# Kernel tuning notes

Hardware: AMD Instinct MI355X
Metric: run time of the kernel (lower is better)

Reference implementation:

```python
import jax, jax.numpy as jnp
from jax import lax
import numpy as np

D_MODEL = 1024
D_STATE = 64
D_CONV = 4
EXPAND = 2
HEADDIM = 64
D_INNER = EXPAND * D_MODEL          # 2048
NHEADS = D_INNER // HEADDIM         # 32
CHUNK = 64
CONV_DIM = D_INNER + 2 * D_STATE    # 2176
D_IN_PROJ = 2 * D_INNER + 2 * D_STATE + NHEADS  # 4256
B_SZ = 4
SEQLEN = 2048
EPS = 1e-5


def _silu(x):
    return x * jax.nn.sigmoid(x)


def _segsum(x):
    # x: [..., T]; returns [..., T, T] with [i,j] = sum_{j<k<=i} x[k], -inf above diag
    T = x.shape[-1]
    xe = jnp.broadcast_to(x[..., None], x.shape + (T,))
    strict_lower = jnp.tril(jnp.ones((T, T), bool), -1)
    xe = jnp.where(strict_lower, xe, 0.0)
    s = jnp.cumsum(xe, axis=-2)
    lower = jnp.tril(jnp.ones((T, T), bool), 0)
    return jnp.where(lower, s, -jnp.inf)


def setup_inputs() -> dict:
    key = jax.random.key(0)
    ks = jax.random.split(key, 5)
    u = jax.random.normal(ks[0], (B_SZ, SEQLEN, D_MODEL), jnp.float32)
    W_in = jax.random.normal(ks[1], (D_IN_PROJ, D_MODEL), jnp.float32) * 0.02
    conv_w = jax.random.normal(ks[2], (CONV_DIM, 1, D_CONV), jnp.float32) * 0.2  # depthwise kernel
    conv_b = jnp.zeros((CONV_DIM,), jnp.float32)
    dt_bias = jax.random.uniform(ks[3], (NHEADS,), jnp.float32, -1.0, 1.0)
    A_log = jnp.log(jnp.linspace(1.0, float(NHEADS), NHEADS)).astype(jnp.float32)
    D = jnp.ones((NHEADS,), jnp.float32)
    norm_w = jnp.ones((D_INNER,), jnp.float32)
    W_out = jax.random.normal(ks[4], (D_MODEL, D_INNER), jnp.float32) * 0.02
    return dict(u=u, W_in=W_in, conv_w=conv_w, conv_b=conv_b, dt_bias=dt_bias,
                A_log=A_log, D=D, norm_w=norm_w, W_out=W_out)


def reference(u, W_in, conv_w, conv_b, dt_bias, A_log, D, norm_w, W_out):
    b, s, _ = u.shape
    A = -jnp.exp(A_log)                                   # [H]
    zxbcdt = u @ W_in.T                                   # [b,s,D_IN_PROJ]
    z = zxbcdt[..., :D_INNER]
    xBC = zxbcdt[..., D_INNER:D_INNER + CONV_DIM]
    dt = jax.nn.softplus(zxbcdt[..., D_INNER + CONV_DIM:] + dt_bias)  # [b,s,H]

    # causal depthwise conv1d (left pad d_conv-1 == torch pad-both + slice[:s])
    xc = lax.conv_general_dilated(
        xBC.transpose(0, 2, 1), conv_w, window_strides=(1,),
        padding=[(D_CONV - 1, 0)], feature_group_count=CONV_DIM,
        dimension_numbers=('NCH', 'OIH', 'NCH'))
    xBC = _silu(xc.transpose(0, 2, 1) + conv_b)           # [b,s,CONV_DIM]

    x = xBC[..., :D_INNER].reshape(b, s, NHEADS, HEADDIM)
    Bm = xBC[..., D_INNER:D_INNER + D_STATE]              # [b,s,N]
    Cm = xBC[..., D_INNER + D_STATE:]                     # [b,s,N]

    # SSD chunked scan
    nch = s // CHUNK
    xs = (x * dt[..., None]).reshape(b, nch, CHUNK, NHEADS, HEADDIM)
    Ad = (A * dt).reshape(b, nch, CHUNK, NHEADS)
    Br = Bm.reshape(b, nch, CHUNK, D_STATE)
    Cr = Cm.reshape(b, nch, CHUNK, D_STATE)
    A_ch = Ad.transpose(0, 1, 3, 2)                       # [b,c,h,l]
    A_cum = jnp.cumsum(A_ch, axis=-1)
    L = jnp.exp(_segsum(A_ch))                            # [b,c,h,l,l]
    Y_diag = jnp.einsum('bcln,bcsn,bchls,bcshp->bclhp', Cr, Br, L, xs)
    decay_states = jnp.exp(A_cum[..., -1:] - A_cum)       # [b,c,h,l]
    states = jnp.einsum('bchl,bcln,bclhp->bchpn', decay_states, Br, xs)
    init = jnp.zeros((b, 1, NHEADS, HEADDIM, D_STATE), xs.dtype)
    states = jnp.concatenate([init, states], axis=1)      # [b,c+1,h,p,n]
    total_decay = jnp.pad(A_cum[..., -1].transpose(0, 2, 1), ((0, 0), (0, 0), (1, 0)))
    decay_chunk = jnp.exp(_segsum(total_decay))           # [b,h,c+1,c+1]
    new_states = jnp.einsum('bhzc,bchpn->bzhpn', decay_chunk, states)
    states = new_states[:, :-1]                           # [b,c,h,p,n]
    state_decay_out = jnp.exp(A_cum)
    Y_off = jnp.einsum('bcln,bchpn,bchl->bclhp', Cr, states, state_decay_out)
    y = (Y_diag + Y_off).reshape(b, s, NHEADS, HEADDIM)

    y = y + x * D[:, None]
    y = y.reshape(b, s, D_INNER)
    # gated RMSNorm
    y = y * _silu(z)
    y = y * lax.rsqrt(jnp.mean(y * y, axis=-1, keepdims=True) + EPS) * norm_w
    return y @ W_out.T
```

## Files before the change

kernel.cpp:

```cpp
#include <hip/hip_runtime.h>
#include <hip/hip_bf16.h>

#define BSZ 4
#define SEQ 2048
#define DMODEL 1024
#define DINNER 2048
#define DSTATE 64
#define NH 32
#define HD 64
#define CKL 64
#define NCH 32
#define CONVD 2176
#define DPROJ 4256
#define N1 4224
#define MTOT 8192
#define YSTR 72

typedef __hip_bfloat16 bf16;
typedef __attribute__((ext_vector_type(8))) short short8;
typedef __attribute__((ext_vector_type(4))) short short4_;
typedef __attribute__((ext_vector_type(4))) float f32x4;

__device__ __forceinline__ float sigmoidf_(float x) { return 1.0f / (1.0f + __expf(-x)); }
__device__ __forceinline__ float bits2f(short s) { return __uint_as_float(((unsigned)(unsigned short)s) << 16); }
__device__ __forceinline__ short f2bits(float f) {
    bf16 h = __float2bfloat16(f);
    return *reinterpret_cast<short*>(&h);
}

__device__ __forceinline__ void gl_lds16(const bf16* g, bf16* l) {
    __builtin_amdgcn_global_load_lds((const __attribute__((address_space(1))) void*)g,
                                     (__attribute__((address_space(3))) void*)l, 16, 0, 0);
}

__device__ __forceinline__ void swz8(int& bx, int& by) {
    int nx = gridDim.x;
    int L = blockIdx.y * nx + blockIdx.x;
    int GSZ = nx * 8;
    int g = L / GSZ, r = L - g * GSZ;
    bx = r % nx;
    by = g * 8 + r / nx;
}

__global__ void k_cvt2(const float* __restrict__ W_in, const float* __restrict__ W_out,
                       const float* __restrict__ nw, bf16* __restrict__ win_b,
                       bf16* __restrict__ wout_b) {
    int g = (blockIdx.x * 256 + threadIdx.x) * 4;
    if (g < N1 * DMODEL) {
        f32x4 f = *(const f32x4*)&W_in[g];
        short4_ o;
#pragma unroll
        for (int j = 0; j < 4; j++) o[j] = f2bits(f[j]);
        *(short4_*)&win_b[g] = o;
    } else if (g < N1 * DMODEL + DMODEL * DINNER) {
        int g2 = g - N1 * DMODEL;
        f32x4 f = *(const f32x4*)&W_out[g2];
        f32x4 w = *(const f32x4*)&nw[g2 & (DINNER - 1)];
        short4_ o;
#pragma unroll
        for (int j = 0; j < 4; j++) o[j] = f2bits(f[j] * w[j]);
        *(short4_*)&wout_b[g2] = o;
    }
}

__global__ __launch_bounds__(256) void k_gemm_bt(const bf16* __restrict__ A, const bf16* __restrict__ W,
                                                 bf16* __restrict__ C, int N, int K, int lda) {
    __shared__ __align__(16) bf16 lA[128 * 64];
    __shared__ __align__(16) bf16 lB[128 * 64];
    const int tid = threadIdx.x;
    const int lane = tid & 63, w = tid >> 6;
    const int wm = w >> 1, wn = w & 1;
    const int lr = lane & 15, lk = lane >> 4;
    int bx, by;
    swz8(bx, by);
    const int m0 = by * 128, n0 = bx * 128;

    f32x4 acc[4][4];
#pragma unroll
    for (int i = 0; i < 4; i++)
#pragma unroll
        for (int j = 0; j < 4; j++) acc[i][j] = (f32x4){0.f, 0.f, 0.f, 0.f};

    const int r = tid >> 3;
    const int cs = ((tid & 7) ^ (r & 7)) * 8;
    const bf16* ga = A + (size_t)(m0 + r) * lda + cs;
    const bf16* gb = W + (size_t)(n0 + r) * K + cs;
    bf16* la0 = lA + tid * 8;
    bf16* lb0 = lB + tid * 8;
    const int sx = (lr & 7);

    for (int kt = 0; kt < K; kt += 64) {
#pragma unroll
        for (int i = 0; i < 4; i++) {
            gl_lds16(ga + kt + (size_t)(32 * i) * lda, la0 + 2048 * i);
            gl_lds16(gb + kt + (size_t)(32 * i) * K, lb0 + 2048 * i);
        }
        __syncthreads();
#pragma unroll
        for (int hh = 0; hh < 2; hh++) {
            const int cb = ((lk + 4 * hh) ^ sx) * 8;
            short8 af[4], bfr[4];
#pragma unroll
            for (int im = 0; im < 4; im++)
                af[im] = *(const short8*)&lA[(wm * 64 + im * 16 + lr) * 64 + cb];
#pragma unroll
            for (int jn = 0; jn < 4; jn++)
                bfr[jn] = *(const short8*)&lB[(wn * 64 + jn * 16 + lr) * 64 + cb];
#pragma unroll
            for (int im = 0; im < 4; im++)
#pragma unroll
                for (int jn = 0; jn < 4; jn++)
                    acc[im][jn] = __builtin_amdgcn_mfma_f32_16x16x32_bf16(af[im], bfr[jn], acc[im][jn], 0, 0, 0);
        }
        __syncthreads();
    }
#pragma unroll
    for (int im = 0; im < 4; im++) {
        int row = m0 + wm * 64 + im * 16 + lk * 4;
#pragma unroll
        for (int jn = 0; jn < 4; jn++) {
            int col = n0 + wn * 64 + jn * 16 + lr;
            bf16* cp = C + (size_t)row * N + col;
#pragma unroll
            for (int rr = 0; rr < 4; rr++) cp[(size_t)rr * N] = __float2bfloat16(acc[im][jn][rr]);
        }
    }
}

__global__ __launch_bounds__(256) void k_gemm2(const bf16* __restrict__ A, const bf16* __restrict__ W,
                                               float* __restrict__ C) {
    __shared__ __align__(16) bf16 lA[128 * 64];
    __shared__ __align__(16) bf16 lB[128 * 64];
    __shared__ float rsrow[128];
    const int tid = threadIdx.x;
    const int lane = tid & 63, w = tid >> 6;
    const int wm = w >> 1, wn = w & 1;
    const int lr = lane & 15, lk = lane >> 4;
    int bx, by;
    swz8(bx, by);
    const int m0 = by * 128, n0 = bx * 128;
    const int K = DINNER, N = DMODEL;

    f32x4 acc[4][4];
#pragma unroll
    for (int i = 0; i < 4; i++)
#pragma unroll
        for (int j = 0; j < 4; j++) acc[i][j] = (f32x4){0.f, 0.f, 0.f, 0.f};
    float ssq[4] = {0.f, 0.f, 0.f, 0.f};

    const int r = tid >> 3;
    const int cs = ((tid & 7) ^ (r & 7)) * 8;
    const bf16* ga = A + (size_t)(m0 + r) * N1 + cs;
    const bf16* gb = W + (size_t)(n0 + r) * K + cs;
    bf16* la0 = lA + tid * 8;
    bf16* lb0 = lB + tid * 8;
    const int sx = (lr & 7);

    for (int kt = 0; kt < K; kt += 64) {
#pragma unroll
        for (int i = 0; i < 4; i++) {
            gl_lds16(ga + kt + (size_t)(32 * i) * N1, la0 + 2048 * i);
            gl_lds16(gb + kt + (size_t)(32 * i) * K, lb0 + 2048 * i);
        }
        __syncthreads();
#pragma unroll
        for (int hh = 0; hh < 2; hh++) {
            const int cb = ((lk + 4 * hh) ^ sx) * 8;
            short8 af[4], bfr[4];
#pragma unroll
            for (int im = 0; im < 4; im++) {
                af[im] = *(const short8*)&lA[(wm * 64 + im * 16 + lr) * 64 + cb];
#pragma unroll
                for (int j = 0; j < 8; j++) { float v = bits2f(af[im][j]); ssq[im] += v * v; }
            }
#pragma unroll
            for (int jn = 0; jn < 4; jn++)
                bfr[jn] = *(const short8*)&lB[(wn * 64 + jn * 16 + lr) * 64 + cb];
#pragma unroll
            for (int im = 0; im < 4; im++)
#pragma unroll
                for (int jn = 0; jn < 4; jn++)
                    acc[im][jn] = __builtin_amdgcn_mfma_f32_16x16x32_bf16(af[im], bfr[jn], acc[im][jn], 0, 0, 0);
        }
        __syncthreads();
    }
#pragma unroll
    for (int im = 0; im < 4; im++) {
        float s = ssq[im];
        s += __shfl_down(s, 32);
        s += __shfl_down(s, 16);
        if (lane < 16) rsrow[wm * 64 + im * 16 + lane] = rsqrtf(s * (1.0f / DINNER) + 1e-5f);
    }
    __syncthreads();
#pragma unroll
    for (int im = 0; im < 4; im++) {
        int rloc = wm * 64 + im * 16 + lk * 4;
        int row = m0 + rloc;
#pragma unroll
        for (int rr = 0; rr < 4; rr++) {
            float s = rsrow[rloc + rr];
#pragma unroll
            for (int jn = 0; jn < 4; jn++) {
                int col = n0 + wn * 64 + jn * 16 + lr;
                C[(size_t)(row + rr) * N + col] = acc[im][jn][rr] * s;
            }
        }
    }
}

__global__ __launch_bounds__(256) void k_prep(const float* __restrict__ u, const float* __restrict__ W_in,
                                              const float* __restrict__ dt_bias,
                                              bf16* __restrict__ u_b, float* __restrict__ dtt) {
    __shared__ __align__(16) float us[8 * DMODEL];
    const int t0 = blockIdx.x * 8;
    const int tid = threadIdx.x;
    const float* ur = u + (size_t)t0 * DMODEL;
    bf16* ub = u_b + (size_t)t0 * DMODEL;
#pragma unroll
    for (int i = 0; i < 8; i++) {
        int idx = (i * 256 + tid) * 4;
        f32x4 v = *(const f32x4*)&ur[idx];
        *(f32x4*)&us[idx] = v;
        short4_ o;
#pragma unroll
        for (int j = 0; j < 4; j++) o[j] = f2bits(v[j]);
        *(short4_*)&ub[idx] = o;
    }
    __syncthreads();
    const int h = tid >> 3, sub = tid & 7;
    const float* wr = W_in + (size_t)(DPROJ - NH + h) * DMODEL;
    float s[8] = {};
    for (int k = sub * 4; k < DMODEL; k += 32) {
        f32x4 w4 = *(const f32x4*)&wr[k];
#pragma unroll
        for (int rr = 0; rr < 8; rr++) {
            const float* up = &us[rr * DMODEL + k];
            s[rr] += up[0] * w4[0] + up[1] * w4[1] + up[2] * w4[2] + up[3] * w4[3];
        }
    }
#pragma unroll
    for (int rr = 0; rr < 8; rr++) {
        s[rr] += __shfl_down(s[rr], 4, 8);
        s[rr] += __shfl_down(s[rr], 2, 8);
        s[rr] += __shfl_down(s[rr], 1, 8);
    }
    if (sub == 0) {
        float bh = dt_bias[h];
#pragma unroll
        for (int rr = 0; rr < 8; rr++) {
            float x = s[rr] + bh;
            dtt[(size_t)h * MTOT + t0 + rr] = (x > 20.f) ? x : log1pf(__expf(x));
        }
    }
}

__global__ void k_conv(const bf16* __restrict__ zx, const float* __restrict__ cw,
                       const float* __restrict__ cb, bf16* __restrict__ xbc) {
    int g = (blockIdx.x * 256 + threadIdx.x) * 4;
    if (g >= MTOT * CONVD) return;
    int c0 = g % CONVD;
    int t = g / CONVD;
    int s = t & (SEQ - 1);
    const short* base = (const short*)(zx + (size_t)t * N1 + DINNER + c0);
    f32x4 w0 = *(const f32x4*)&cw[(c0 + 0) * 4];
    f32x4 w1 = *(const f32x4*)&cw[(c0 + 1) * 4];
    f32x4 w2 = *(const f32x4*)&cw[(c0 + 2) * 4];
    f32x4 w3 = *(const f32x4*)&cw[(c0 + 3) * 4];
    f32x4 a = *(const f32x4*)&cb[c0];
#pragma unroll
    for (int k = 0; k < 4; k++) {
        int st = s - 3 + k;
        if (st >= 0) {
            short4_ v = *(const short4_*)(base + (long)(k - 3) * N1);
            a[0] += bits2f(v[0]) * w0[k];
            a[1] += bits2f(v[1]) * w1[k];
            a[2] += bits2f(v[2]) * w2[k];
            a[3] += bits2f(v[3]) * w3[k];
        }
    }
    short4_ o;
#pragma unroll
    for (int j = 0; j < 4; j++) o[j] = f2bits(a[j] * sigmoidf_(a[j]));
    *(short4_*)&xbc[g] = o;
}

__global__ __launch_bounds__(256) void k_ssd(const bf16* __restrict__ xbc, const float* __restrict__ dtt,
                                             const float* __restrict__ A_log, const float* __restrict__ Dp,
                                             bf16* __restrict__ zx) {
    __shared__ __align__(16) short Ct[2][64 * YSTR];
    __shared__ __align__(16) short Bt[2][64 * YSTR];
    __shared__ __align__(16) short Bn[2][64 * YSTR];
    __shared__ __align__(16) short Xt[2][32 * YSTR];
    __shared__ __align__(16) short Sb[2][32 * YSTR];
    __shared__ __align__(16) short Gs[4 * 16 * YSTR];
    __shared__ __align__(16) float Sf[32 * 68];
    __shared__ __align__(16) float sdt2[2][64], sAc2[2][64], sf2[2][64];
    __shared__ float set2[2];

    const int ph = blockIdx.x, h = blockIdx.y, b = blockIdx.z;
    const int tid = threadIdx.x;
    const int lane = tid & 63, w = tid >> 6;
    const int lr = lane & 15, lk = lane >> 4;
    const float Ah = -__expf(A_log[h]);
    const float Dh = Dp[h];
    const int xcol = h * HD + ph * 32;

    const int lrow = tid >> 2, c0 = (tid & 3) * 16, px = (tid & 3) * 8;
    const int zl = 16 * w + (lane >> 2), zp = (lane & 3) * 8;

    short8 rC0, rC1, rB0, rB1, rX, rZ;
    float rdt;
    auto load_chunk = [&](int cc) {
        int rows0 = b * SEQ + cc * CKL;
        const short* rp = (const short*)(xbc + (size_t)(rows0 + lrow) * CONVD);
        rC0 = *(const short8*)&rp[DINNER + DSTATE + c0];
        rC1 = *(const short8*)&rp[DINNER + DSTATE + c0 + 8];
        rB0 = *(const short8*)&rp[DINNER + c0];
        rB1 = *(const short8*)&rp[DINNER + c0 + 8];
        rX  = *(const short8*)&rp[xcol + px];
        rZ  = *(const short8*)((const short*)zx + (size_t)(rows0 + zl) * N1 + xcol + zp);
        rdt = dtt[(size_t)h * MTOT + rows0 + lane];
    };
    auto scatter = [&](int buf) {
        *(short8*)&Ct[buf][lrow * YSTR + c0] = rC0;
        *(short8*)&Ct[buf][lrow * YSTR + c0 + 8] = rC1;
        *(short8*)&Bt[buf][lrow * YSTR + c0] = rB0;
        *(short8*)&Bt[buf][lrow * YSTR + c0 + 8] = rB1;
#pragma unroll
        for (int j = 0; j < 8; j++) {
            Bn[buf][(c0 + j) * YSTR + lrow] = rB0[j];
            Bn[buf][(c0 + 8 + j) * YSTR + lrow] = rB1[j];
            Xt[buf][(px + j) * YSTR + lrow] = rX[j];
        }
    };
    auto dtscan = [&](int buf) {
        if (tid < 64) {
            float dv = rdt;
            float v = Ah * dv;
#pragma unroll
            for (int d = 1; d < 64; d <<= 1) { float o = __shfl_up(v, d); if (tid >= d) v += o; }
            float tot = __shfl(v, 63);
            sdt2[buf][tid] = dv; sAc2[buf][tid] = v; sf2[buf][tid] = __expf(tot - v) * dv;
            if (tid == 63) set2[buf] = __expf(tot);
        }
    };

    for (int i = tid; i < 32 * 68; i += 256) Sf[i] = 0.f;
    for (int i = tid; i < 32 * YSTR; i += 256) Sb[0][i] = 0;
    load_chunk(0);
    scatter(0);
    dtscan(0);
    __syncthreads();

    for (int c = 0; c < NCH; c++) {
        const int par = c & 1, nb = par ^ 1;
        const int rows0 = b * SEQ + c * CKL;
        float etot = set2[par];
        short8 zcur = rZ;
        if (c + 1 < NCH) load_chunk(c + 1);

        short8 cf0 = *(const short8*)&Ct[par][(16 * w + lr) * YSTR + lk * 8];
        short8 cf1 = *(const short8*)&Ct[par][(16 * w + lr) * YSTR + 32 + lk * 8];
        f32x4 acc[2];
#pragma unroll
        for (int t = 0; t < 2; t++) {
            short8 s0 = *(const short8*)&Sb[par][(16 * t + lr) * YSTR + lk * 8];
            short8 s1 = *(const short8*)&Sb[par][(16 * t + lr) * YSTR + 32 + lk * 8];
            acc[t] = __builtin_amdgcn_mfma_f32_16x16x32_bf16(cf0, s0, (f32x4){0.f, 0.f, 0.f, 0.f}, 0, 0, 0);
            acc[t] = __builtin_amdgcn_mfma_f32_16x16x32_bf16(cf1, s1, acc[t], 0, 0, 0);
        }
        float sAcl[4], el[4];
#pragma unroll
        for (int rr = 0; rr < 4; rr++) { sAcl[rr] = sAc2[par][16 * w + lk * 4 + rr]; el[rr] = __expf(sAcl[rr]); }
#pragma unroll
        for (int t = 0; t < 2; t++)
#pragma unroll
            for (int rr = 0; rr < 4; rr++) acc[t][rr] *= el[rr];
        short* gw = Gs + w * 16 * YSTR;
#pragma unroll
        for (int t = 0; t < 4; t++) {
            short8 b0 = *(const short8*)&Bt[par][(16 * t + lr) * YSTR + lk * 8];
            short8 b1 = *(const short8*)&Bt[par][(16 * t + lr) * YSTR + 32 + lk * 8];
            f32x4 g = __builtin_amdgcn_mfma_f32_16x16x32_bf16(cf0, b0, (f32x4){0.f, 0.f, 0.f, 0.f}, 0, 0, 0);
            g = __builtin_amdgcn_mfma_f32_16x16x32_bf16(cf1, b1, g, 0, 0, 0);
            int s = 16 * t + lr;
            float sAcs = sAc2[par][s], dts = sdt2[par][s];
#pragma unroll
            for (int rr = 0; rr < 4; rr++) {
                int l = 16 * w + lk * 4 + rr;
                float v = (s <= l) ? g[rr] * __expf(sAcl[rr] - sAcs) * dts : 0.f;
                gw[(lk * 4 + rr) * YSTR + s] = f2bits(v);
            }
        }
        short8 gf0 = *(const short8*)&gw[lr * YSTR + lk * 8];
        short8 gf1 = *(const short8*)&gw[lr * YSTR + 32 + lk * 8];
#pragma unroll
        for (int t = 0; t < 2; t++) {
            short8 x0 = *(const short8*)&Xt[par][(16 * t + lr) * YSTR + lk * 8];
            short8 x1 = *(const short8*)&Xt[par][(16 * t + lr) * YSTR + 32 + lk * 8];
            acc[t] = __builtin_amdgcn_mfma_f32_16x16x32_bf16(gf0, x0, acc[t], 0, 0, 0);
            acc[t] = __builtin_amdgcn_mfma_f32_16x16x32_bf16(gf1, x1, acc[t], 0, 0, 0);
        }
        {
            int pw = w & 1, nh2 = w >> 1;
            short8 xt0 = *(const short8*)&Xt[par][(16 * pw + lr) * YSTR + lk * 8];
            short8 xt1 = *(const short8*)&Xt[par][(16 * pw + lr) * YSTR + 32 + lk * 8];
            f32x4 sa0 = *(const f32x4*)&sf2[par][lk * 8];
            f32x4 sa1 = *(const f32x4*)&sf2[par][lk * 8 + 4];
            f32x4 sb0 = *(const f32x4*)&sf2[par][32 + lk * 8];
            f32x4 sb1 = *(const f32x4*)&sf2[par][32 + lk * 8 + 4];
            short8 xd0, xd1;
#pragma unroll
            for (int j = 0; j < 4; j++) {
                xd0[j]     = f2bits(bits2f(xt0[j])     * sa0[j]);
                xd0[4 + j] = f2bits(bits2f(xt0[4 + j]) * sa1[j]);
                xd1[j]     = f2bits(bits2f(xt1[j])     * sb0[j]);
                xd1[4 + j] = f2bits(bits2f(xt1[4 + j]) * sb1[j]);
            }
#pragma unroll
            for (int j = 0; j < 2; j++) {
                int nt = 2 * nh2 + j;
                short8 b0 = *(const short8*)&Bn[par][(16 * nt + lr) * YSTR + lk * 8];
                short8 b1 = *(const short8*)&Bn[par][(16 * nt + lr) * YSTR + 32 + lk * 8];
                f32x4 sacc = __builtin_amdgcn_mfma_f32_16x16x32_bf16(xd0, b0, (f32x4){0.f, 0.f, 0.f, 0.f}, 0, 0, 0);
                sacc = __builtin_amdgcn_mfma_f32_16x16x32_bf16(xd1, b1, sacc, 0, 0, 0);
#pragma unroll
                for (int rr = 0; rr < 4; rr++) {
                    int n = 16 * nt + lr;
                    int p = 16 * pw + lk * 4 + rr;
                    float nv = Sf[p * 68 + n] * etot + sacc[rr];
                    Sf[p * 68 + n] = nv;
                    Sb[nb][p * YSTR + n] = f2bits(nv);
                }
            }
        }
#pragma unroll
        for (int t = 0; t < 2; t++) {
#pragma unroll
            for (int rr = 0; rr < 4; rr++) {
                int p = 16 * t + lr;
                int l = 16 * w + lk * 4 + rr;
                float y = acc[t][rr] + Dh * bits2f(Xt[par][p * YSTR + l]);
                Ct[par][l * YSTR + p] = f2bits(y);
            }
        }
        {
            short8 y8 = *(const short8*)&Ct[par][zl * YSTR + zp];
            short* zpp = (short*)zx + (size_t)(rows0 + zl) * N1 + xcol + zp;
            short8 o;
#pragma unroll
            for (int j = 0; j < 8; j++) {
                float z = bits2f(zcur[j]);
                o[j] = f2bits(bits2f(y8[j]) * (z * sigmoidf_(z)));
            }
            *(short8*)zpp = o;
        }
        if (c + 1 < NCH) {
            scatter(nb);
            dtscan(nb);
        }
        __syncthreads();
    }
}

extern "C" void kernel_launch(void* const* d_in, const int* in_sizes, int n_in,
                              void* d_out, int out_size, void* d_ws, size_t ws_size,
                              hipStream_t stream) {
    const float* u       = (const float*)d_in[0];
    const float* W_in    = (const float*)d_in[1];
    const float* conv_w  = (const float*)d_in[2];
    const float* conv_b  = (const float*)d_in[3];
    const float* dt_bias = (const float*)d_in[4];
    const float* A_log   = (const float*)d_in[5];
    const float* Dp      = (const float*)d_in[6];
    const float* norm_w  = (const float*)d_in[7];
    const float* W_out   = (const float*)d_in[8];
    float* out = (float*)d_out;

    char* ws = (char*)d_ws;
    bf16* zx     = (bf16*)ws;  ws += (size_t)MTOT * N1 * 2;
    bf16* xbc    = (bf16*)ws;  ws += (size_t)MTOT * CONVD * 2;
    bf16* wout_b = (bf16*)ws;  ws += (size_t)DMODEL * DINNER * 2;
    float* dtt   = (float*)ws; ws += (size_t)NH * MTOT * 4;

    bf16* u_b   = (bf16*)d_out;
    bf16* win_b = (bf16*)((char*)d_out + (size_t)MTOT * DMODEL * 2);

    k_prep<<<MTOT / 8, 256, 0, stream>>>(u, W_in, dt_bias, u_b, dtt);
    k_cvt2<<<((N1 * DMODEL + DMODEL * DINNER) / 4 + 255) / 256, 256, 0, stream>>>(
        W_in, W_out, norm_w, win_b, wout_b);

    k_gemm_bt<<<dim3(N1 / 128, MTOT / 128), 256, 0, stream>>>(u_b, win_b, zx, N1, DMODEL, DMODEL);

    k_conv<<<(MTOT * CONVD / 4 + 255) / 256, 256, 0, stream>>>(zx, conv_w, conv_b, xbc);

    k_ssd<<<dim3(2, NH, BSZ), 256, 0, stream>>>(xbc, dtt, A_log, Dp, zx);

    k_gemm2<<<dim3(DMODEL / 128, MTOT / 128), 256, 0, stream>>>(zx, wout_b, out);
}
```

Measured before the change: 407.7 us.

## Replace both GEMMs with 8-wave double-buffered pipelined MFMA template kernel

Replaces the two 128x128 single-buffered GEMM kernels with one templated 512-thread kernel. It uses wider N tiles (384 for the input projection, 256 for the output projection), double-buffered LDS split into half-K stages, and async global-to-LDS loads issued ahead of compute with explicit vmcnt waits. MFMA clusters run under raised priority with sched barriers, and the tile order changes to an XCD-aware block remap. The goal is to hide global load latency and raise MFMA utilisation. In exchange it brings larger LDS use, hand-tuned wait counts that are easy to get wrong, and fewer blocks per GEMM.

```diff
diff --git a/kernel.cpp b/kernel.cpp
--- a/kernel.cpp
+++ b/kernel.cpp
@@ -33,13 +33,26 @@
                                      (__attribute__((address_space(3))) void*)l, 16, 0, 0);
 }
 
-__device__ __forceinline__ void swz8(int& bx, int& by) {
-    int nx = gridDim.x;
-    int L = blockIdx.y * nx + blockIdx.x;
-    int GSZ = nx * 8;
-    int g = L / GSZ, r = L - g * GSZ;
-    bx = r % nx;
-    by = g * 8 + r / nx;
+__device__ __forceinline__ f32x4 MF(short8 a, short8 b, f32x4 c) {
+    return __builtin_amdgcn_mfma_f32_16x16x32_bf16(a, b, c, 0, 0, 0);
+}
+
+template<int N> __device__ __forceinline__ void vmw() {
+    if constexpr (N < 0) {}
+    else if constexpr (N == 0)  asm volatile("s_waitcnt vmcnt(0)" ::: "memory");
+    else if constexpr (N == 1)  asm volatile("s_waitcnt vmcnt(1)" ::: "memory");
+    else if constexpr (N == 2)  asm volatile("s_waitcnt vmcnt(2)" ::: "memory");
+    else if constexpr (N == 3)  asm volatile("s_waitcnt vmcnt(3)" ::: "memory");
+    else if constexpr (N == 4)  asm volatile("s_waitcnt vmcnt(4)" ::: "memory");
+    else if constexpr (N == 5)  asm volatile("s_waitcnt vmcnt(5)" ::: "memory");
+    else if constexpr (N == 6)  asm volatile("s_waitcnt vmcnt(6)" ::: "memory");
+    else if constexpr (N == 7)  asm volatile("s_waitcnt vmcnt(7)" ::: "memory");
+    else if constexpr (N == 8)  asm volatile("s_waitcnt vmcnt(8)" ::: "memory");
+    else if constexpr (N == 9)  asm volatile("s_waitcnt vmcnt(9)" ::: "memory");
+    else if constexpr (N == 10) asm volatile("s_waitcnt vmcnt(10)" ::: "memory");
+    else if constexpr (N == 11) asm volatile("s_waitcnt vmcnt(11)" ::: "memory");
+    else if constexpr (N == 12) asm volatile("s_waitcnt vmcnt(12)" ::: "memory");
+    else                        asm volatile("s_waitcnt vmcnt(15)" ::: "memory");
 }
 
 __global__ void k_cvt2(const float* __restrict__ W_in, const float* __restrict__ W_out,
@@ -63,146 +76,171 @@
     }
 }
 
-__global__ __launch_bounds__(256) void k_gemm_bt(const bf16* __restrict__ A, const bf16* __restrict__ W,
-                                                 bf16* __restrict__ C, int N, int K, int lda) {
-    __shared__ __align__(16) bf16 lA[128 * 64];
-    __shared__ __align__(16) bf16 lB[128 * 64];
+template<int BN, int NT, int LDA, int LDC, bool RMS, typename CT>
+__global__ __launch_bounds__(512, 2) void k_mm8(const bf16* __restrict__ Ap,
+                                                const bf16* __restrict__ Wp,
+                                                CT* __restrict__ Cp) {
+    constexpr int K   = NT * 64;
+    constexpr int NJ  = BN / 64;
+    constexpr int WNW = BN / 4;
+    constexpr int LB  = BN / 128;
+    constexpr int SBH = BN * 32;
+    constexpr int WS  = 3 * LB + 2;
+
+    __shared__ __align__(16) short SA[16384];
+    __shared__ __align__(16) short SB[4 * SBH];
+    __shared__ float rsrow[RMS ? 128 : 1];
+
     const int tid = threadIdx.x;
     const int lane = tid & 63, w = tid >> 6;
-    const int wm = w >> 1, wn = w & 1;
+    const int wm = w >> 2, wn = w & 3;
     const int lr = lane & 15, lk = lane >> 4;
-    int bx, by;
-    swz8(bx, by);
-    const int m0 = by * 128, n0 = bx * 128;
-
-    f32x4 acc[4][4];
+
+    const int NX = gridDim.x;
+    {
+    }
+    int L = blockIdx.y * NX + blockIdx.x;
+    int nwg = NX * gridDim.y;
+    int Lx = (L & 7) * (nwg >> 3) + (L >> 3);
+    const int m0 = (Lx / NX) * 128, n0 = (Lx % NX) * BN;
+
+    const int la = tid >> 2;
+    const int rA = (la & ~5) | ((la & 1) << 2) | ((la >> 2) & 1);
+    const bf16* pA = Ap + (size_t)(m0 + rA) * LDA + (((tid & 3) ^ (rA & 3)) * 8);
+    const bf16* pB[LB];
+#pragma unroll
+    for (int q = 0; q < LB; q++) {
+        int lb = (w * LB + q) * 16 + (lane >> 2);
+        int rB = (lb & ~5) | ((lb & 1) << 2) | ((lb >> 2) & 1);
+        pB[q] = Wp + (size_t)(n0 + rB) * K + (((lane & 3) ^ (rB & 3)) * 8);
+    }
+
+    auto stA = [&](int d, int h, int t) {
+        gl_lds16(pA + t * 64 + h * 32, (bf16*)&SA[(d * 2 + h) * 4096 + tid * 8]);
+    };
+    auto stB = [&](int d, int h, int t) {
+#pragma unroll
+        for (int q = 0; q < LB; q++)
+            gl_lds16(pB[q] + t * 64 + h * 32,
+                     (bf16*)&SB[(d * 2 + h) * SBH + (w * LB + q) * 512 + lane * 8]);
+    };
+
+    const int lnsw = (lr & 10) | ((lr & 1) << 2) | ((lr >> 2) & 1);
+    const int pe = (lk ^ (lr & 3)) * 8;
+    const int aBase = (wm * 64 + lnsw) * 32 + pe;
+    const int bBase = (wn * WNW + lnsw) * 32 + pe;
+
+    f32x4 acc[4][NJ];
 #pragma unroll
     for (int i = 0; i < 4; i++)
 #pragma unroll
-        for (int j = 0; j < 4; j++) acc[i][j] = (f32x4){0.f, 0.f, 0.f, 0.f};
-
-    const int r = tid >> 3;
-    const int cs = ((tid & 7) ^ (r & 7)) * 8;
-    const bf16* ga = A + (size_t)(m0 + r) * lda + cs;
-    const bf16* gb = W + (size_t)(n0 + r) * K + cs;
-    bf16* la0 = lA + tid * 8;
-    bf16* lb0 = lB + tid * 8;
-    const int sx = (lr & 7);
-
-    for (int kt = 0; kt < K; kt += 64) {
+        for (int j = 0; j < NJ; j++) acc[i][j] = (f32x4){0.f, 0.f, 0.f, 0.f};
+    float ssq[4] = {0.f, 0.f, 0.f, 0.f};
+
+#define CLUSTER(I0, I1)                                              \
+    do {                                                             \
+        __builtin_amdgcn_s_barrier();                                \
+        asm volatile("s_waitcnt lgkmcnt(0)" ::: "memory");           \
+        __builtin_amdgcn_sched_barrier(0);                           \
+        __builtin_amdgcn_s_setprio(1);                               \
+        _Pragma("unroll")                                            \
+        for (int j = 0; j < NJ; ++j) {                               \
+            acc[I0][j] = MF(af[0], bfr[j], acc[I0][j]);              \
+            acc[I1][j] = MF(af[1], bfr[j], acc[I1][j]);              \
+        }                                                            \
+        __builtin_amdgcn_s_setprio(0);                               \
+    } while (0)
+
+#define SSQ2(I0, I1)                                                 \
+    if constexpr (RMS) {                                             \
+        _Pragma("unroll")                                            \
+        for (int e = 0; e < 8; ++e) {                                \
+            float v0 = bits2f(af[0][e]), v1 = bits2f(af[1][e]);      \
+            ssq[I0] += v0 * v0; ssq[I1] += v1 * v1;                  \
+        }                                                            \
+    }
+
+    stB(0, 0, 0); stA(0, 0, 0); stB(0, 1, 0); stA(0, 1, 0);
+    stB(1, 0, 1); stA(1, 0, 1); stB(1, 1, 1);
+    vmw<WS>();
+    __builtin_amdgcn_s_barrier();
+
+#pragma unroll
+    for (int t = 0; t < NT; ++t) {
+        const int d = t & 1;
+        const int A0 = d * 8192, A1 = A0 + 4096;
+        const int B0 = d * 2 * SBH, B1 = B0 + SBH;
+        short8 af[2], bfr[NJ];
+#pragma unroll
+        for (int j = 0; j < NJ; ++j) bfr[j] = *(const short8*)&SB[B0 + bBase + j * 512];
+        af[0] = *(const short8*)&SA[A0 + aBase];
+        af[1] = *(const short8*)&SA[A0 + aBase + 512];
+        if (t + 1 < NT) stA(d ^ 1, 1, t + 1);
+        CLUSTER(0, 1);
+        SSQ2(0, 1);
+        __builtin_amdgcn_s_barrier();
+        af[0] = *(const short8*)&SA[A0 + aBase + 1024];
+        af[1] = *(const short8*)&SA[A0 + aBase + 1536];
+        if (t + 2 < NT) stB(d, 0, t + 2);
+        CLUSTER(2, 3);
+        SSQ2(2, 3);
+        if (t < NT - 2) vmw<WS>();
+        else if (t == NT - 2) vmw<2 * LB + 2>();
+        else vmw<0>();
+        __builtin_amdgcn_s_barrier();
+#pragma unroll
+        for (int j = 0; j < NJ; ++j) bfr[j] = *(const short8*)&SB[B1 + bBase + j * 512];
+        af[0] = *(const short8*)&SA[A1 + aBase];
+        af[1] = *(const short8*)&SA[A1 + aBase + 512];
+        if (t + 2 < NT) stA(d, 0, t + 2);
+        CLUSTER(0, 1);
+        SSQ2(0, 1);
+        __builtin_amdgcn_s_barrier();
+        af[0] = *(const short8*)&SA[A1 + aBase + 1024];
+        af[1] = *(const short8*)&SA[A1 + aBase + 1536];
+        if (t + 2 < NT) stB(d, 1, t + 2);
+        CLUSTER(2, 3);
+        SSQ2(2, 3);
+        if (t < NT - 2) vmw<WS>();
+        else if (t == NT - 2) vmw<LB + 1>();
+        __builtin_amdgcn_s_barrier();
+    }
+#undef CLUSTER
+#undef SSQ2
+
+    if constexpr (RMS) {
 #pragma unroll
         for (int i = 0; i < 4; i++) {
-            gl_lds16(ga + kt + (size_t)(32 * i) * lda, la0 + 2048 * i);
-            gl_lds16(gb + kt + (size_t)(32 * i) * K, lb0 + 2048 * i);
+            float s = ssq[i];
+            s += __shfl_down(s, 32);
+            s += __shfl_down(s, 16);
+            if (lane < 16) rsrow[wm * 64 + i * 16 + lane] = rsqrtf(s * (1.0f / DINNER) + 1e-5f);
         }
         __syncthreads();
 #pragma unroll
-        for (int hh = 0; hh < 2; hh++) {
-            const int cb = ((lk + 4 * hh) ^ sx) * 8;
-            short8 af[4], bfr[4];
-#pragma unroll
-            for (int im = 0; im < 4; im++)
-                af[im] = *(const short8*)&lA[(wm * 64 + im * 16 + lr) * 64 + cb];
-#pragma unroll
-            for (int jn = 0; jn < 4; jn++)
-                bfr[jn] = *(const short8*)&lB[(wn * 64 + jn * 16 + lr) * 64 + cb];
-#pragma unroll
-            for (int im = 0; im < 4; im++)
-#pragma unroll
-                for (int jn = 0; jn < 4; jn++)
-                    acc[im][jn] = __builtin_amdgcn_mfma_f32_16x16x32_bf16(af[im], bfr[jn], acc[im][jn], 0, 0, 0);
-        }
-        __syncthreads();
-    }
-#pragma unroll
-    for (int im = 0; im < 4; im++) {
-        int row = m0 + wm * 64 + im * 16 + lk * 4;
-#pragma unroll
-        for (int jn = 0; jn < 4; jn++) {
-            int col = n0 + wn * 64 + jn * 16 + lr;
-            bf16* cp = C + (size_t)row * N + col;
-#pragma unroll
-            for (int rr = 0; rr < 4; rr++) cp[(size_t)rr * N] = __float2bfloat16(acc[im][jn][rr]);
-        }
-    }
-}
-
-__global__ __launch_bounds__(256) void k_gemm2(const bf16* __restrict__ A, const bf16* __restrict__ W,
-                                               float* __restrict__ C) {
-    __shared__ __align__(16) bf16 lA[128 * 64];
-    __shared__ __align__(16) bf16 lB[128 * 64];
-    __shared__ float rsrow[128];
-    const int tid = threadIdx.x;
-    const int lane = tid & 63, w = tid >> 6;
-    const int wm = w >> 1, wn = w & 1;
-    const int lr = lane & 15, lk = lane >> 4;
-    int bx, by;
-    swz8(bx, by);
-    const int m0 = by * 128, n0 = bx * 128;
-    const int K = DINNER, N = DMODEL;
-
-    f32x4 acc[4][4];
-#pragma unroll
-    for (int i = 0; i < 4; i++)
-#pragma unroll
-        for (int j = 0; j < 4; j++) acc[i][j] = (f32x4){0.f, 0.f, 0.f, 0.f};
-    float ssq[4] = {0.f, 0.f, 0.f, 0.f};
-
-    const int r = tid >> 3;
-    const int cs = ((tid & 7) ^ (r & 7)) * 8;
-    const bf16* ga = A + (size_t)(m0 + r) * N1 + cs;
-    const bf16* gb = W + (size_t)(n0 + r) * K + cs;
-    bf16* la0 = lA + tid * 8;
-    bf16* lb0 = lB + tid * 8;
-    const int sx = (lr & 7);
-
-    for (int kt = 0; kt < K; kt += 64) {
-#pragma unroll
         for (int i = 0; i < 4; i++) {
-            gl_lds16(ga + kt + (size_t)(32 * i) * N1, la0 + 2048 * i);
-            gl_lds16(gb + kt + (size_t)(32 * i) * K, lb0 + 2048 * i);
-        }
-        __syncthreads();
-#pragma unroll
-        for (int hh = 0; hh < 2; hh++) {
-            const int cb = ((lk + 4 * hh) ^ sx) * 8;
-            short8 af[4], bfr[4];
-#pragma unroll
-            for (int im = 0; im < 4; im++) {
-                af[im] = *(const short8*)&lA[(wm * 64 + im * 16 + lr) * 64 + cb];
-#pragma unroll
-                for (int j = 0; j < 8; j++) { float v = bits2f(af[im][j]); ssq[im] += v * v; }
-            }
-#pragma unroll
-            for (int jn = 0; jn < 4; jn++)
-                bfr[jn] = *(const short8*)&lB[(wn * 64 + jn * 16 + lr) * 64 + cb];
-#pragma unroll
-            for (int im = 0; im < 4; im++)
-#pragma unroll
-                for (int jn = 0; jn < 4; jn++)
-                    acc[im][jn] = __builtin_amdgcn_mfma_f32_16x16x32_bf16(af[im], bfr[jn], acc[im][jn], 0, 0, 0);
-        }
-        __syncthreads();
-    }
-#pragma unroll
-    for (int im = 0; im < 4; im++) {
-        float s = ssq[im];
-        s += __shfl_down(s, 32);
-        s += __shfl_down(s, 16);
-        if (lane < 16) rsrow[wm * 64 + im * 16 + lane] = rsqrtf(s * (1.0f / DINNER) + 1e-5f);
-    }
-    __syncthreads();
-#pragma unroll
-    for (int im = 0; im < 4; im++) {
-        int rloc = wm * 64 + im * 16 + lk * 4;
-        int row = m0 + rloc;
-#pragma unroll
-        for (int rr = 0; rr < 4; rr++) {
-            float s = rsrow[rloc + rr];
-#pragma unroll
-            for (int jn = 0; jn < 4; jn++) {
-                int col = n0 + wn * 64 + jn * 16 + lr;
-                C[(size_t)(row + rr) * N + col] = acc[im][jn][rr] * s;
+            int rl = wm * 64 + i * 16 + lk * 4;
+            int row = m0 + rl;
+#pragma unroll
+            for (int rr = 0; rr < 4; rr++) {
+                float s = rsrow[rl + rr];
+#pragma unroll
+                for (int j = 0; j < NJ; j++) {
+                    int col = n0 + wn * WNW + j * 16 + lr;
+                    Cp[(size_t)(row + rr) * LDC + col] = acc[i][j][rr] * s;
+                }
+            }
+        }
+    } else {
+#pragma unroll
+        for (int i = 0; i < 4; i++) {
+            int row = m0 + wm * 64 + i * 16 + lk * 4;
+#pragma unroll
+            for (int j = 0; j < NJ; j++) {
+                int col = n0 + wn * WNW + j * 16 + lr;
+                bf16* cp = (bf16*)Cp + (size_t)row * LDC + col;
+#pragma unroll
+                for (int rr = 0; rr < 4; rr++) cp[(size_t)rr * LDC] = __float2bfloat16(acc[i][j][rr]);
             }
         }
     }
@@ -490,11 +528,13 @@
     k_cvt2<<<((N1 * DMODEL + DMODEL * DINNER) / 4 + 255) / 256, 256, 0, stream>>>(
         W_in, W_out, norm_w, win_b, wout_b);
 
-    k_gemm_bt<<<dim3(N1 / 128, MTOT / 128), 256, 0, stream>>>(u_b, win_b, zx, N1, DMODEL, DMODEL);
+    k_mm8<384, 16, DMODEL, N1, false, bf16>
+        <<<dim3(N1 / 384, MTOT / 128), 512, 0, stream>>>(u_b, win_b, zx);
 
     k_conv<<<(MTOT * CONVD / 4 + 255) / 256, 256, 0, stream>>>(zx, conv_w, conv_b, xbc);
 
     k_ssd<<<dim3(2, NH, BSZ), 256, 0, stream>>>(xbc, dtt, A_log, Dp, zx);
 
-    k_gemm2<<<dim3(DMODEL / 128, MTOT / 128), 256, 0, stream>>>(zx, wout_b, out);
-}
+    k_mm8<256, 32, N1, DMODEL, true, float>
+        <<<dim3(DMODEL / 256, MTOT / 128), 512, 0, stream>>>(zx, wout_b, out);
+}
```

New measurement: 556.4 us. +36.5%, slower.
